# Kernel tuning notes

Hardware: AMD Instinct MI355X
Metric: run time of the kernel (lower is better)

The kernel has to match this reference:

```python
import jax, jax.numpy as jnp
import numpy as np

EPS = 1e-4      # geomloss: eps = blur**p = 0.01**2
N_ITERS = 20    # fixed Sinkhorn iterations
UNI_T = 2.0     # uniformity temperature (Wang & Isola)


def _sqdist(x, y):
    # [N,D],[M,D] -> [N,M] squared euclidean distances
    return jnp.sum((x[:, None, :] - y[None, :, :]) ** 2, axis=-1)


def _cost(x, y):
    # geomloss p=2 cost: ||x-y||^2 / 2
    return 0.5 * _sqdist(x, y)


def _softmin(C, h):
    # f_i = -eps * log( (1/M) * sum_j exp((h_j - C_ij)/eps) )
    M = C.shape[1]
    lse = jax.nn.logsumexp((h[None, :] - C) / EPS, axis=1)
    return -EPS * (lse - jnp.log(jnp.float32(M)))


def _sinkhorn_potentials(C):
    # alternating log-domain Sinkhorn updates, uniform weights
    def body(carry, _):
        f, g = carry
        f = _softmin(C, g)
        g = _softmin(C.T, f)
        return (f, g), None
    init = (jnp.zeros(C.shape[0], C.dtype), jnp.zeros(C.shape[1], C.dtype))
    (f, g), _ = jax.lax.scan(body, init, None, length=N_ITERS)
    return f, g


def _sym_potential(C):
    # symmetric fixed-point for the debiasing terms OT_eps(a,a)
    def body(p, _):
        return 0.5 * (p + _softmin(C, p)), None
    p, _ = jax.lax.scan(body, jnp.zeros(C.shape[0], C.dtype), None, length=N_ITERS)
    return p


def sinkhorn_divergence(x, y):
    # debiased: S = OT(x,y) - 0.5*OT(x,x) - 0.5*OT(y,y); envelope-theorem grads
    Cxy = _cost(x, y)
    f_d, g_d = _sinkhorn_potentials(jax.lax.stop_gradient(Cxy))
    f = _softmin(Cxy, jax.lax.stop_gradient(g_d))          # final differentiable step
    g = _softmin(Cxy.T, jax.lax.stop_gradient(f_d))

    Cxx = _cost(x, x)
    px = _sym_potential(jax.lax.stop_gradient(Cxx))
    fx = _softmin(Cxx, jax.lax.stop_gradient(px))          # 0.5*OT(x,x) = mean(fx)

    Cyy = _cost(y, y)
    py = _sym_potential(jax.lax.stop_gradient(Cyy))
    fy = _softmin(Cyy, jax.lax.stop_gradient(py))

    return jnp.mean(f) + jnp.mean(g) - jnp.mean(fx) - jnp.mean(fy)


def uniformity(x):
    # log E_{i != j} [ exp(-t * ||x_i - x_j||^2) ]
    N = x.shape[0]
    D = _sqdist(x, x)
    D = D + jnp.diag(jnp.full((N,), jnp.inf, dtype=x.dtype))  # mask self-pairs
    return jax.nn.logsumexp(-UNI_T * D) - jnp.log(jnp.float32(N * (N - 1)))


def setup_inputs() -> dict:
    key = jax.random.key(0)
    k1, k2 = jax.random.split(key)
    p_q = jax.random.normal(k1, (4096, 3), dtype=jnp.float32)
    p_gt = jax.random.normal(k2, (4096, 4), dtype=jnp.float32)
    return {"p_q": p_q, "p_gt": p_gt}


def reference(p_q, p_gt):
    L = sinkhorn_divergence(p_q, p_gt[:, :3])
    L = L + uniformity(p_q)
    return L
```

## Files before the change

### kernel.cpp

```cpp
#include <hip/hip_runtime.h>

#define NPT  4096
#define NBLK 256
#define NTHR 1024

constexpr float EPSV   = 1e-4f;
constexpr float LN2F   = 0.69314718055994531f;
constexpr float E2     = EPSV * LN2F;
constexpr float INV_E2 = 1.0f / E2;
constexpr float S_U    = 4.0f / LN2F;

#define SMEM_FLOATS 33024
#define SMEM_BYTES  (SMEM_FLOATS * 4)

typedef float v2f __attribute__((ext_vector_type(2)));

__device__ __forceinline__ float fexp2(float x) { return __builtin_amdgcn_exp2f(x); }
__device__ __forceinline__ float flog2(float x) { return __builtin_amdgcn_logf(x); }

__device__ __forceinline__ v2f pk_fma(v2f a, v2f b, v2f c) {
    v2f d;
    asm("v_pk_fma_f32 %0, %1, %2, %3" : "=v"(d) : "v"(a), "v"(b), "v"(c));
    return d;
}
__device__ __forceinline__ v2f pk_add(v2f a, v2f b) {
    v2f d;
    asm("v_pk_add_f32 %0, %1, %2" : "=v"(d) : "v"(a), "v"(b));
    return d;
}
__device__ __forceinline__ float max3f(float a, float b, float c) {
    float d;
    asm("v_max3_f32 %0, %1, %2, %3" : "=v"(d) : "v"(a), "v"(b), "v"(c));
    return d;
}

__device__ __forceinline__ float gload(const float* p) {
    return __hip_atomic_load(p, __ATOMIC_RELAXED, __HIP_MEMORY_SCOPE_SYSTEM);
}
__device__ __forceinline__ void gstore(float* p, float v) {
    __hip_atomic_store(p, v, __ATOMIC_RELAXED, __HIP_MEMORY_SCOPE_SYSTEM);
}

__device__ __forceinline__ void group_barrier(unsigned* base, unsigned target, int b) {
    asm volatile("s_waitcnt vmcnt(0)" ::: "memory");
    __syncthreads();
    if (threadIdx.x == 0) {
        __hip_atomic_fetch_add(&base[(b & 15) * 16], 1u,
                               __ATOMIC_RELAXED, __HIP_MEMORY_SCOPE_SYSTEM);
        for (;;) {
            unsigned tot = 0;
#pragma unroll
            for (int i = 0; i < 16; ++i)
                tot += __hip_atomic_load(&base[i * 16],
                                         __ATOMIC_RELAXED, __HIP_MEMORY_SCOPE_SYSTEM);
            if (tot >= target) break;
            __builtin_amdgcn_s_sleep(1);
        }
    }
    __syncthreads();
}

template<bool ISU>
__device__ __forceinline__ void run_task(
    const float4* __restrict__ cpA, const float4* __restrict__ cpB,
    const float*  __restrict__ rAf, const float*  __restrict__ rBf,
    int r0g, int half, int lane, float scale, float2* part, int lr0)
{
    v2f xs0[2], xs1[2], xs2[2];
#pragma unroll
    for (int r = 0; r < 2; ++r) {
        const int rr = r0g + r;
        const int pb4 = (rr >> 1) * 4, c0 = rr & 1;
        float xv = rAf[pb4 + c0] * scale;
        float yv = rAf[pb4 + 2 + c0] * scale;
        float zv = rBf[pb4 + c0] * scale;
        xs0[r].x = xv; xs0[r].y = xv;
        xs1[r].x = yv; xs1[r].y = yv;
        xs2[r].x = zv; xs2[r].y = zv;
    }
    float m[2], s[2];
    const int pbase = half * 1024 + lane;
    const float4* colA = cpA + pbase;
    const float4* colB = cpB + pbase;

#pragma unroll
    for (int chunk = 0; chunk < 4; ++chunk) {
        v2f av[2][4];
        float mc[2] = {-1e30f, -1e30f};
#pragma unroll
        for (int k = 0; k < 4; ++k) {
            const float4 a4 = colA[(chunk * 4 + k) * 64];
            const float4 b4 = colB[(chunk * 4 + k) * 64];
            v2f xx; xx.x = a4.x; xx.y = a4.y;
            v2f yy; yy.x = a4.z; yy.y = a4.w;
            v2f zz; zz.x = b4.x; zz.y = b4.y;
            v2f gg; gg.x = b4.z; gg.y = b4.w;
#pragma unroll
            for (int r = 0; r < 2; ++r) {
                v2f a01 = pk_fma(xs2[r], zz, gg);
                a01 = pk_fma(xs1[r], yy, a01);
                a01 = pk_fma(xs0[r], xx, a01);
                if (ISU) {
                    const int p = pbase + (chunk * 4 + k) * 64;
                    const int rr = r0g + r;
                    if (p == (rr >> 1)) {
                        if (rr & 1) a01.y = -1e30f; else a01.x = -1e30f;
                    }
                }
                av[r][k] = a01;
                mc[r] = max3f(mc[r], a01.x, a01.y);
            }
        }
#pragma unroll
        for (int r = 0; r < 2; ++r) {
            const float nm = -mc[r];
            v2f mcn; mcn.x = nm; mcn.y = nm;
            float sA = 0.0f, sB = 0.0f;
#pragma unroll
            for (int k = 0; k < 4; ++k) {
                v2f d = pk_add(av[r][k], mcn);
                sA += fexp2(d.x);
                sB += fexp2(d.y);
            }
            const float sc_ = sA + sB;
            if (chunk == 0) { m[r] = mc[r]; s[r] = sc_; }
            else {
                float dd = m[r] - mc[r];
                float e = fexp2(-fabsf(dd));
                float bigs   = (dd >= 0.0f) ? s[r] : sc_;
                float smalls = (dd >= 0.0f) ? sc_  : s[r];
                s[r] = fmaf(smalls, e, bigs);
                m[r] = fmaxf(m[r], mc[r]);
            }
        }
    }
    float ml[2] = {m[0], m[1]};
#pragma unroll
    for (int off = 1; off < 64; off <<= 1) {
#pragma unroll
        for (int r = 0; r < 2; ++r)
            m[r] = fmaxf(m[r], __shfl_xor(m[r], off, 64));
    }
#pragma unroll
    for (int r = 0; r < 2; ++r) s[r] *= fexp2(ml[r] - m[r]);
#pragma unroll
    for (int off = 1; off < 64; off <<= 1) {
#pragma unroll
        for (int r = 0; r < 2; ++r)
            s[r] += __shfl_xor(s[r], off, 64);
    }
    if (lane == 0) {
        part[(lr0 + 0) * 2 + half] = make_float2(m[0], s[0]);
        part[(lr0 + 1) * 2 + half] = make_float2(m[1], s[1]);
    }
}

__global__ void sink_init(float* __restrict__ ws) {
    int t = blockIdx.x * blockDim.x + threadIdx.x;
    if (t < NPT) {
        gstore(ws + t, 0.0f);
        gstore(ws + 4096 + t, 0.0f);
        gstore(ws + 8192 + t, 0.0f);
        gstore(ws + 16384 + t, 0.0f);
    }
    if (t < 512) {
        __hip_atomic_store((unsigned*)(ws + 40960) + t, 0u,
                           __ATOMIC_RELAXED, __HIP_MEMORY_SCOPE_SYSTEM);
    }
}

__global__ __launch_bounds__(NTHR)
__attribute__((amdgpu_waves_per_eu(4, 4)))
void sink_main(
    const float* __restrict__ xin, const float* __restrict__ yin,
    float* __restrict__ ws, float* __restrict__ out)
{
    extern __shared__ float smem[];
    float4* pAx = (float4*)smem;
    float4* pBx = (float4*)(smem + 8192);
    float4* pAy = (float4*)(smem + 16384);
    float4* pBy = (float4*)(smem + 24576);
    float2* part = (float2*)(smem + 32768);

    float* f    = ws;
    float* g    = ws + 4096;
    float* px0  = ws + 8192;
    float* px1  = ws + 12288;
    float* py0  = ws + 16384;
    float* py1  = ws + 20480;
    float* ffin = ws + 24576;
    float* fxv  = ws + 28672;
    float* fyv  = ws + 32768;
    float* uls  = ws + 36864;
    unsigned* ctrA = (unsigned*)(ws + 40960);
    unsigned* ctrB = (unsigned*)(ws + 40960) + 256;

    const int tid  = threadIdx.x;
    const int b    = blockIdx.x;
    const int wave = tid >> 6;
    const int lane = tid & 63;
    unsigned* cbarrier = (b < 128) ? ctrA : ctrB;

    const float4* yin4 = (const float4*)yin;
    for (int i = tid; i < 2048; i += NTHR) {
        float x0 = xin[6 * i + 0], y0v = xin[6 * i + 1], z0 = xin[6 * i + 2];
        float x1 = xin[6 * i + 3], y1v = xin[6 * i + 4], z1 = xin[6 * i + 5];
        pAx[i] = make_float4(x0, x1, y0v, y1v);
        pBx[i] = make_float4(z0, z1, 0.0f, 0.0f);
        float4 v0 = yin4[2 * i], v1 = yin4[2 * i + 1];
        pAy[i] = make_float4(v0.x, v1.x, v0.y, v1.y);
        pBy[i] = make_float4(v0.z, v1.z, 0.0f, 0.0f);
    }
    __syncthreads();

    for (int h = 0; h <= 40; ++h) {
        bool rows_x, cols_x, isU = false, avg = false;
        const float* pot; float* outp; float scale = INV_E2;
        int row0g, rows_pb;
        if (h == 0) {
            if (b < 128)      { rows_x = true;  cols_x = false; pot = g;    outp = f;    rows_pb = 32; row0g = b * 32; }
            else if (b < 192) { rows_x = true;  cols_x = true;  pot = px0;  outp = px1;  avg = true; rows_pb = 64; row0g = (b - 128) * 64; }
            else              { rows_x = true;  cols_x = true;  pot = nullptr; outp = uls; isU = true; scale = S_U; rows_pb = 64; row0g = (b - 192) * 64; }
        } else if (h == 40) {
            if (b < 128)      { rows_x = true;  cols_x = false; pot = g;    outp = ffin; rows_pb = 32; row0g = b * 32; }
            else if (b < 192) { rows_x = true;  cols_x = true;  pot = px0;  outp = fxv;  rows_pb = 64; row0g = (b - 128) * 64; }
            else              { rows_x = false; cols_x = false; pot = py0;  outp = fyv;  rows_pb = 64; row0g = (b - 192) * 64; }
        } else if (h & 1) {
            int k = (h - 1) >> 1;
            if (b < 128) { rows_x = false; cols_x = true;  pot = f; outp = g; rows_pb = 32; row0g = b * 32; }
            else         { rows_x = false; cols_x = false; pot = (k & 1) ? py1 : py0; outp = (k & 1) ? py0 : py1; avg = true; rows_pb = 32; row0g = (b - 128) * 32; }
        } else {
            int k = h >> 1;
            if (b < 128) { rows_x = true; cols_x = false; pot = g; outp = f; rows_pb = 32; row0g = b * 32; }
            else         { rows_x = true; cols_x = true;  pot = (k & 1) ? px1 : px0; outp = (k & 1) ? px0 : px1; avg = true; rows_pb = 32; row0g = (b - 128) * 32; }
        }

        float4* cpA = cols_x ? pAx : pAy;
        float4* cpB = cols_x ? pBx : pBy;
        for (int p = tid; p < 2048; p += NTHR) {
            float4 a4 = cpA[p];
            float4 b4 = cpB[p];
            float cn0 = 0.5f * (a4.x * a4.x + a4.z * a4.z + b4.x * b4.x);
            float cn1 = 0.5f * (a4.y * a4.y + a4.w * a4.w + b4.y * b4.y);
            float pv0 = pot ? gload(pot + 2 * p)     : 0.0f;
            float pv1 = pot ? gload(pot + 2 * p + 1) : 0.0f;
            ((float2*)&cpB[p])[1] = make_float2((pv0 - cn0) * scale,
                                                (pv1 - cn1) * scale);
        }
        __syncthreads();

        const float* rAf = (const float*)(rows_x ? pAx : pAy);
        const float* rBf = (const float*)(rows_x ? pBx : pBy);
        const int ntask = rows_pb;
        for (int t = wave; t < ntask; t += 16) {
            int grp = t >> 1, half = t & 1;
            int lr0 = grp << 1;
            int r0g = row0g + lr0;
            if (isU) run_task<true >(cpA, cpB, rAf, rBf, r0g, half, lane, scale, part, lr0);
            else     run_task<false>(cpA, cpB, rAf, rBf, r0g, half, lane, scale, part, lr0);
        }
        __syncthreads();

        if (tid < rows_pb) {
            float2 pa = part[tid * 2 + 0], pb = part[tid * 2 + 1];
            float mm = fmaxf(pa.x, pb.x);
            float ss = pa.y * fexp2(pa.x - mm) + pb.y * fexp2(pb.x - mm);
            int rg = row0g + tid;
            const int pb4 = (rg >> 1) * 4, c0 = rg & 1;
            float xv = rAf[pb4 + c0];
            float yv = rAf[pb4 + 2 + c0];
            float zv = rBf[pb4 + c0];
            float rn = 0.5f * (xv * xv + yv * yv + zv * zv);
            float lse2 = mm + flog2(ss) - rn * scale;
            float val;
            if (isU) {
                val = lse2;
            } else {
                val = -E2 * (lse2 - 12.0f);
                if (avg) val = 0.5f * (gload(pot + rg) + val);
            }
            gstore(outp + rg, val);
        }

        group_barrier(cbarrier, 128u * (unsigned)(h + 1), b);
    }

    if (b == 0) {
        if (tid == 0) {
            for (;;) {
                unsigned tot = 0;
#pragma unroll
                for (int i = 0; i < 16; ++i)
                    tot += __hip_atomic_load(&ctrB[i * 16],
                                             __ATOMIC_RELAXED, __HIP_MEMORY_SCOPE_SYSTEM);
                if (tot >= 128u * 41u) break;
                __builtin_amdgcn_s_sleep(1);
            }
        }
        __syncthreads();

        float sf = 0.f, sg = 0.f, sx = 0.f, sy = 0.f, um = -1e30f, us = 0.f;
        for (int i = tid; i < NPT; i += NTHR) {
            sf += gload(ffin + i); sg += gload(g + i);
            sx += gload(fxv + i);  sy += gload(fyv + i);
            float v = gload(uls + i);
            float mn = fmaxf(um, v);
            us = us * fexp2(um - mn) + fexp2(v - mn);
            um = mn;
        }
#pragma unroll
        for (int off = 1; off < 64; off <<= 1) {
            sf += __shfl_xor(sf, off, 64);
            sg += __shfl_xor(sg, off, 64);
            sx += __shfl_xor(sx, off, 64);
            sy += __shfl_xor(sy, off, 64);
            float mo = __shfl_xor(um, off, 64);
            float so = __shfl_xor(us, off, 64);
            float mn = fmaxf(um, mo);
            us = us * fexp2(um - mn) + so * fexp2(mo - mn);
            um = mn;
        }
        __syncthreads();
        if (lane == 0) {
            float* red = smem;
            red[wave * 6 + 0] = sf; red[wave * 6 + 1] = sg; red[wave * 6 + 2] = sx;
            red[wave * 6 + 3] = sy; red[wave * 6 + 4] = um; red[wave * 6 + 5] = us;
        }
        __syncthreads();
        if (tid == 0) {
            float* red = smem;
            float Sf = 0, Sg = 0, Sx = 0, Sy = 0, Um = -1e30f, Us = 0;
            for (int w = 0; w < 16; ++w) {
                Sf += red[w * 6 + 0]; Sg += red[w * 6 + 1];
                Sx += red[w * 6 + 2]; Sy += red[w * 6 + 3];
                float mo = red[w * 6 + 4], so = red[w * 6 + 5];
                float mn = fmaxf(Um, mo);
                Us = Us * fexp2(Um - mn) + so * fexp2(mo - mn);
                Um = mn;
            }
            float mean = (Sf + Sg - Sx - Sy) * (1.0f / 4096.0f);
            float U = LN2F * (Um + flog2(Us)) - logf(4096.0f * 4095.0f);
            out[0] = mean + U;
        }
    }
}

extern "C" void kernel_launch(void* const* d_in, const int* in_sizes, int n_in,
                              void* d_out, int out_size, void* d_ws, size_t ws_size,
                              hipStream_t stream) {
    const float* x = (const float*)d_in[0];
    const float* y = (const float*)d_in[1];
    float* ws  = (float*)d_ws;
    float* out = (float*)d_out;

    (void)hipFuncSetAttribute((const void*)sink_main,
                              hipFuncAttributeMaxDynamicSharedMemorySize, SMEM_BYTES);

    sink_init<<<4, 1024, 0, stream>>>(ws);
    sink_main<<<NBLK, NTHR, SMEM_BYTES, stream>>>(x, y, ws, out);
}
```

Measured before the change: 535.3 us.

## Process four rows per wave with online LSE and DPP partial reductions

Each wave task now covers four row pairs instead of two, so every column load from LDS is reused across more rows. The chunked max-then-exp pass becomes a per-element online logsumexp, which takes three exp2 per element instead of roughly two. The 64-lane shuffle reduction is replaced by three DPP steps within 8-lane groups, which writes 16 partials per row into a larger shared buffer that the final pass merges. The goal is fewer cross-lane shuffles and better load reuse, paid for with extra exp work, more registers, and fewer tasks per block.

```diff
diff --git a/kernel.cpp b/kernel.cpp
--- a/kernel.cpp
+++ b/kernel.cpp
@@ -10,7 +10,7 @@
 constexpr float INV_E2 = 1.0f / E2;
 constexpr float S_U    = 4.0f / LN2F;
 
-#define SMEM_FLOATS 33024
+#define SMEM_FLOATS 34816
 #define SMEM_BYTES  (SMEM_FLOATS * 4)
 
 typedef float v2f __attribute__((ext_vector_type(2)));
@@ -23,15 +23,16 @@
     asm("v_pk_fma_f32 %0, %1, %2, %3" : "=v"(d) : "v"(a), "v"(b), "v"(c));
     return d;
 }
-__device__ __forceinline__ v2f pk_add(v2f a, v2f b) {
-    v2f d;
-    asm("v_pk_add_f32 %0, %1, %2" : "=v"(d) : "v"(a), "v"(b));
-    return d;
-}
 __device__ __forceinline__ float max3f(float a, float b, float c) {
     float d;
     asm("v_max3_f32 %0, %1, %2, %3" : "=v"(d) : "v"(a), "v"(b), "v"(c));
     return d;
+}
+
+template<int CTRL>
+__device__ __forceinline__ float dppf(float x) {
+    return __int_as_float(__builtin_amdgcn_update_dpp(
+        __float_as_int(x), __float_as_int(x), CTRL, 0xF, 0xF, false));
 }
 
 __device__ __forceinline__ float gload(const float* p) {
@@ -64,94 +65,67 @@
 __device__ __forceinline__ void run_task(
     const float4* __restrict__ cpA, const float4* __restrict__ cpB,
     const float*  __restrict__ rAf, const float*  __restrict__ rBf,
-    int r0g, int half, int lane, float scale, float2* part, int lr0)
+    int r0g, int half, int lane, float scale, float2* part2, int lr0)
 {
-    v2f xs0[2], xs1[2], xs2[2];
-#pragma unroll
-    for (int r = 0; r < 2; ++r) {
+    v2f xs0[4], xs1[4], xs2[4];
+#pragma unroll
+    for (int r = 0; r < 4; ++r) {
         const int rr = r0g + r;
         const int pb4 = (rr >> 1) * 4, c0 = rr & 1;
         float xv = rAf[pb4 + c0] * scale;
         float yv = rAf[pb4 + 2 + c0] * scale;
         float zv = rBf[pb4 + c0] * scale;
-        xs0[r].x = xv; xs0[r].y = xv;
-        xs1[r].x = yv; xs1[r].y = yv;
-        xs2[r].x = zv; xs2[r].y = zv;
-    }
-    float m[2], s[2];
+        xs0[r] = (v2f){xv, xv};
+        xs1[r] = (v2f){yv, yv};
+        xs2[r] = (v2f){zv, zv};
+    }
+    float m[4] = {-1e30f, -1e30f, -1e30f, -1e30f};
+    float s[4] = {0.0f, 0.0f, 0.0f, 0.0f};
+
     const int pbase = half * 1024 + lane;
     const float4* colA = cpA + pbase;
     const float4* colB = cpB + pbase;
 
 #pragma unroll
-    for (int chunk = 0; chunk < 4; ++chunk) {
-        v2f av[2][4];
-        float mc[2] = {-1e30f, -1e30f};
-#pragma unroll
-        for (int k = 0; k < 4; ++k) {
-            const float4 a4 = colA[(chunk * 4 + k) * 64];
-            const float4 b4 = colB[(chunk * 4 + k) * 64];
-            v2f xx; xx.x = a4.x; xx.y = a4.y;
-            v2f yy; yy.x = a4.z; yy.y = a4.w;
-            v2f zz; zz.x = b4.x; zz.y = b4.y;
-            v2f gg; gg.x = b4.z; gg.y = b4.w;
-#pragma unroll
-            for (int r = 0; r < 2; ++r) {
-                v2f a01 = pk_fma(xs2[r], zz, gg);
-                a01 = pk_fma(xs1[r], yy, a01);
-                a01 = pk_fma(xs0[r], xx, a01);
-                if (ISU) {
-                    const int p = pbase + (chunk * 4 + k) * 64;
-                    const int rr = r0g + r;
-                    if (p == (rr >> 1)) {
-                        if (rr & 1) a01.y = -1e30f; else a01.x = -1e30f;
-                    }
+    for (int i = 0; i < 16; ++i) {
+        const float4 a4 = colA[i * 64];
+        const float4 b4 = colB[i * 64];
+        const v2f xx = {a4.x, a4.y}, yy = {a4.z, a4.w};
+        const v2f zz = {b4.x, b4.y}, gg = {b4.z, b4.w};
+#pragma unroll
+        for (int r = 0; r < 4; ++r) {
+            v2f a01 = pk_fma(xs2[r], zz, gg);
+            a01 = pk_fma(xs1[r], yy, a01);
+            a01 = pk_fma(xs0[r], xx, a01);
+            if (ISU) {
+                const int p = pbase + i * 64;
+                const int rr = r0g + r;
+                if (p == (rr >> 1)) {
+                    if (rr & 1) a01.y = -1e30f; else a01.x = -1e30f;
                 }
-                av[r][k] = a01;
-                mc[r] = max3f(mc[r], a01.x, a01.y);
-            }
-        }
-#pragma unroll
-        for (int r = 0; r < 2; ++r) {
-            const float nm = -mc[r];
-            v2f mcn; mcn.x = nm; mcn.y = nm;
-            float sA = 0.0f, sB = 0.0f;
-#pragma unroll
-            for (int k = 0; k < 4; ++k) {
-                v2f d = pk_add(av[r][k], mcn);
-                sA += fexp2(d.x);
-                sB += fexp2(d.y);
-            }
-            const float sc_ = sA + sB;
-            if (chunk == 0) { m[r] = mc[r]; s[r] = sc_; }
-            else {
-                float dd = m[r] - mc[r];
-                float e = fexp2(-fabsf(dd));
-                float bigs   = (dd >= 0.0f) ? s[r] : sc_;
-                float smalls = (dd >= 0.0f) ? sc_  : s[r];
-                s[r] = fmaf(smalls, e, bigs);
-                m[r] = fmaxf(m[r], mc[r]);
-            }
-        }
-    }
-    float ml[2] = {m[0], m[1]};
-#pragma unroll
-    for (int off = 1; off < 64; off <<= 1) {
-#pragma unroll
-        for (int r = 0; r < 2; ++r)
-            m[r] = fmaxf(m[r], __shfl_xor(m[r], off, 64));
-    }
-#pragma unroll
-    for (int r = 0; r < 2; ++r) s[r] *= fexp2(ml[r] - m[r]);
-#pragma unroll
-    for (int off = 1; off < 64; off <<= 1) {
-#pragma unroll
-        for (int r = 0; r < 2; ++r)
-            s[r] += __shfl_xor(s[r], off, 64);
-    }
-    if (lane == 0) {
-        part[(lr0 + 0) * 2 + half] = make_float2(m[0], s[0]);
-        part[(lr0 + 1) * 2 + half] = make_float2(m[1], s[1]);
+            }
+            const float mnew = max3f(m[r], a01.x, a01.y);
+            const float es = fexp2(m[r] - mnew);
+            const float e0 = fexp2(a01.x - mnew);
+            const float e1 = fexp2(a01.y - mnew);
+            s[r] = fmaf(s[r], es, e0 + e1);
+            m[r] = mnew;
+        }
+    }
+
+#pragma unroll
+    for (int r = 0; r < 4; ++r) {
+        const float ml = m[r];
+        float mm = m[r];
+        mm = fmaxf(mm, dppf<0xB1>(mm));
+        mm = fmaxf(mm, dppf<0x4E>(mm));
+        mm = fmaxf(mm, dppf<0x141>(mm));
+        float ssv = s[r] * fexp2(ml - mm);
+        ssv += dppf<0xB1>(ssv);
+        ssv += dppf<0x4E>(ssv);
+        ssv += dppf<0x141>(ssv);
+        if ((lane & 7) == 0)
+            part2[(lr0 + r) * 16 + half * 8 + (lane >> 3)] = make_float2(mm, ssv);
     }
 }
 
@@ -180,7 +154,7 @@
     float4* pBx = (float4*)(smem + 8192);
     float4* pAy = (float4*)(smem + 16384);
     float4* pBy = (float4*)(smem + 24576);
-    float2* part = (float2*)(smem + 32768);
+    float2* part2 = (float2*)(smem + 32768);
 
     float* f    = ws;
     float* g    = ws + 4096;
@@ -251,20 +225,25 @@
 
         const float* rAf = (const float*)(rows_x ? pAx : pAy);
         const float* rBf = (const float*)(rows_x ? pBx : pBy);
-        const int ntask = rows_pb;
+        const int ntask = rows_pb >> 1;
         for (int t = wave; t < ntask; t += 16) {
             int grp = t >> 1, half = t & 1;
-            int lr0 = grp << 1;
+            int lr0 = grp << 2;
             int r0g = row0g + lr0;
-            if (isU) run_task<true >(cpA, cpB, rAf, rBf, r0g, half, lane, scale, part, lr0);
-            else     run_task<false>(cpA, cpB, rAf, rBf, r0g, half, lane, scale, part, lr0);
+            if (isU) run_task<true >(cpA, cpB, rAf, rBf, r0g, half, lane, scale, part2, lr0);
+            else     run_task<false>(cpA, cpB, rAf, rBf, r0g, half, lane, scale, part2, lr0);
         }
         __syncthreads();
 
         if (tid < rows_pb) {
-            float2 pa = part[tid * 2 + 0], pb = part[tid * 2 + 1];
-            float mm = fmaxf(pa.x, pb.x);
-            float ss = pa.y * fexp2(pa.x - mm) + pb.y * fexp2(pb.x - mm);
+            float mm = -1e30f, ss = 0.0f;
+#pragma unroll
+            for (int q = 0; q < 16; ++q) {
+                float2 p2 = part2[tid * 16 + q];
+                float mn = fmaxf(mm, p2.x);
+                ss = ss * fexp2(mm - mn) + p2.y * fexp2(p2.x - mn);
+                mm = mn;
+            }
             int rg = row0g + tid;
             const int pb4 = (rg >> 1) * 4, c0 = rg & 1;
             float xv = rAf[pb4 + c0];
```

New measurement: 1.216 ms. 127% more time.
